# Performance work log

Measured on AMD Instinct MI355X. Metric: run time of the kernel, lower is better.

Reference implementation:

```python
import jax, jax.numpy as jnp
import numpy as np

NUM_JOINT_TYPES = 17
SINKHORN_ITERS = 50
TAU = 0.05
LAMBDA_RES = 0.5
LLOYD_ITERS = 10


def _sqdist(a, b):
    # squared euclidean distances [n, m] (== torch.cdist(...,p=2)**2)
    d = jnp.sum(a * a, -1)[:, None] + jnp.sum(b * b, -1)[None, :] - 2.0 * (a @ b.T)
    return jnp.maximum(d, 0.0)


def _kmeans_centroids(key, positions, k):
    # k-means++ init followed by LLOYD_ITERS Lloyd steps; result is a fixed
    # spatial prior (detached in the original), so stop_gradient at the end.
    n = positions.shape[0]
    key, k0 = jax.random.split(key)
    i0 = jax.random.randint(k0, (), 0, n)
    cents = jnp.zeros((k, 2), positions.dtype).at[0].set(positions[i0])

    def pp_body(i, carry):
        cents, key = carry
        key, sub = jax.random.split(key)
        d = _sqdist(positions, cents)                       # [n, k]
        d = jnp.where(jnp.arange(k)[None, :] < i, d, jnp.inf)
        dmin = jnp.min(d, axis=1)
        probs = dmin / (jnp.sum(dmin) + 1e-8)
        idx = jax.random.categorical(sub, jnp.log(probs + 1e-12))
        return cents.at[i].set(positions[idx]), key

    cents, _ = jax.lax.fori_loop(1, k, pp_body, (cents, key))

    def lloyd_body(_, cents):
        assign = jnp.argmin(_sqdist(positions, cents), axis=1)  # [n]
        sums = jax.ops.segment_sum(positions, assign, num_segments=k)
        counts = jax.ops.segment_sum(jnp.ones((n,), positions.dtype), assign, num_segments=k)
        means = sums / jnp.maximum(counts, 1.0)[:, None]
        return jnp.where((counts > 0)[:, None], means, cents)

    cents = jax.lax.fori_loop(0, LLOYD_ITERS, lloyd_body, cents)
    return jax.lax.stop_gradient(cents)


def _sinkhorn(cost, n, k):
    # log-domain Sinkhorn-Knopp with one slack column
    n_slots = k * NUM_JOINT_TYPES
    log_K_ext = jnp.concatenate([-cost / TAU, jnp.zeros((n, 1), cost.dtype)], axis=1)
    tgt = jnp.ones((n_slots + 1,), cost.dtype).at[-1].set(float(max(n - n_slots, 1)))
    log_tgt = jnp.log(tgt)

    def step(carry, _):
        log_u, log_v = carry
        log_u = -jax.scipy.special.logsumexp(log_K_ext + log_v[None, :], axis=1)
        log_v = log_tgt - jax.scipy.special.logsumexp(log_K_ext + log_u[:, None], axis=0)
        return (log_u, log_v), None

    init = (jnp.zeros((n,), cost.dtype), jnp.zeros((n_slots + 1,), cost.dtype))
    (log_u, log_v), _ = jax.lax.scan(jax.checkpoint(step), init, None, length=SINKHORN_ITERS)
    T = jnp.exp(log_K_ext + log_u[:, None] + log_v[None, :])
    return T[:, :n_slots]


def setup_inputs() -> dict:
    key = jax.random.key(0)
    k1, k2, k3, k4, k5 = jax.random.split(key, 5)
    N, D, H, K_MAX, K = 20000, 256, 128, 128, 64
    emb = jax.random.normal(k1, (N, D), jnp.float32)
    emb = emb / jnp.linalg.norm(emb, axis=-1, keepdims=True)  # L2-normalised per docstring
    positions = jax.random.uniform(k2, (N, 2), jnp.float32)
    W1 = jax.random.normal(k3, (D, H), jnp.float32) / np.sqrt(D)
    b1 = jnp.zeros((H,), jnp.float32)
    prototype_pool = jax.random.normal(k4, (K_MAX, H), jnp.float32) * 0.5
    joint_types = jax.random.randint(k5, (N,), 0, NUM_JOINT_TYPES, jnp.int32)
    return {"embeddings": emb, "positions": positions, "W1": W1, "b1": b1,
            "prototype_pool": prototype_pool, "joint_types": joint_types, "k": K}


def reference(embeddings, positions, W1, b1, prototype_pool, joint_types, k):
    n = embeddings.shape[0]
    h = jax.nn.selu(embeddings @ W1 + b1)                    # node_encoder
    prototypes = prototype_pool[:k]                          # k <= k_max branch
    c_learned = _sqdist(h, prototypes)                       # [n, k]
    centroids = _kmeans_centroids(jax.random.key(42), positions, k)
    c_spatial = _sqdist(positions, centroids)                # [n, k]
    cost_pp = c_spatial + LAMBDA_RES * c_learned
    cost = jnp.repeat(cost_pp, NUM_JOINT_TYPES, axis=1)      # [n, k*17]
    slot_types = jnp.tile(jnp.arange(NUM_JOINT_TYPES), k)
    type_mask = joint_types[:, None] == slot_types[None, :]
    cost = jnp.where(type_mask, cost, 1e6)
    T = _sinkhorn(cost, n, k)                                # [n, k*17]
    logits = jnp.log(T.reshape(n, k, NUM_JOINT_TYPES).sum(axis=2) + 1e-8)
    return logits, T
```

## Files before the change

### kernel.cpp

```cpp
#include <hip/hip_runtime.h>

#define NPT 20000
#define DIMK 256
#define HD 128
#define KC 64
#define NT 17
#define NSLOT (KC*NT)
#define SINK_IT 50
#define NBLK 250
#define RPB 80
#define LGB 64
#define CPB 313

#define OFF_H     0
#define OFF_CL    (NPT*HD)
#define OFF_Q     (OFF_CL + NPT*KC)
#define OFF_LS    (OFF_Q + KC*NPT)
#define OFF_LOGU  (OFF_LS + NPT*KC)
#define OFF_ORDER (OFF_LOGU + NPT)
#define OFF_TSV   (OFF_ORDER + NPT)
#define OFF_OFFS  (OFF_TSV + NPT)
#define OFF_CENTS (OFF_OFFS + 32)
#define OFF_I0    (OFF_CENTS + 128)
#define OFF_SUB   (OFF_I0 + 32)
#define OFF_LLP   (OFF_SUB + 128)
#define OFF_PMB   (OFF_LLP + LGB*192)
#define OFF_PSB   (OFF_PMB + NBLK*3*64)
#define OFF_RUNT  (OFF_PSB + NBLK*3*64)
#define OFF_PLM   (OFF_RUNT + 768)
#define OFF_PLS   (OFF_PLM + 256)

__device__ __forceinline__ void tf2x32(unsigned k0, unsigned k1,
                                       unsigned x0, unsigned x1,
                                       unsigned& o0, unsigned& o1) {
  unsigned ks0 = k0, ks1 = k1, ks2 = k0 ^ k1 ^ 0x1BD11BDAu;
  x0 += ks0; x1 += ks1;
  const int rot[2][4] = {{13,15,26,6},{17,29,16,24}};
  unsigned ks[3] = {ks0, ks1, ks2};
  #pragma unroll
  for (int i = 0; i < 5; ++i) {
    #pragma unroll
    for (int r = 0; r < 4; ++r) {
      int rr = rot[i & 1][r];
      x0 += x1;
      x1 = (x1 << rr) | (x1 >> (32 - rr));
      x1 ^= x0;
    }
    x0 += ks[(i+1)%3];
    x1 += ks[(i+2)%3] + (unsigned)(i+1);
  }
  o0 = x0; o1 = x1;
}

__device__ __forceinline__ void lse_merge(float& m, float& s, float m2, float s2) {
  float mn = fmaxf(m, m2);
  s = s*__expf(m - mn) + s2*__expf(m2 - mn);
  m = mn;
}

__global__ void k_keys(unsigned* sub, int* i0p) {
  if (threadIdx.x != 0 || blockIdx.x != 0) return;
  unsigned key0 = 0u, key1 = 42u;
  unsigned c0, c1, s0, s1;
  tf2x32(key0, key1, 0u, 0u, c0, c1);
  tf2x32(key0, key1, 0u, 1u, s0, s1);
  key0 = c0; key1 = c1;
  unsigned k1a, k1b, k2a, k2b;
  tf2x32(s0, s1, 0u, 0u, k1a, k1b);
  tf2x32(s0, s1, 0u, 1u, k2a, k2b);
  unsigned h0, h1, l0, l1;
  tf2x32(k1a, k1b, 0u, 0u, h0, h1);
  tf2x32(k2a, k2b, 0u, 0u, l0, l1);
  unsigned hb = h0 ^ h1, lb = l0 ^ l1;
  unsigned span = 20000u;
  unsigned m1 = 65536u % span;
  unsigned mult = (unsigned)(((unsigned long long)m1 * m1) % span);
  unsigned off32 = (hb % span) * mult + (lb % span);
  *i0p = (int)(off32 % span);
  sub[0] = 0u; sub[1] = 0u;
  for (int i = 1; i < KC; ++i) {
    tf2x32(key0, key1, 0u, 0u, c0, c1);
    tf2x32(key0, key1, 0u, 1u, s0, s1);
    key0 = c0; key1 = c1;
    sub[2*i] = s0; sub[2*i+1] = s1;
  }
}

__global__ __launch_bounds__(256) void k_gumbel(const unsigned* __restrict__ sub,
                                                float* __restrict__ Q) {
  int s = blockIdx.y + 1;
  int i = blockIdx.x * 256 + threadIdx.x;
  if (i >= NPT) return;
  unsigned o0, o1;
  tf2x32(sub[2*s], sub[2*s+1], 0u, (unsigned)i, o0, o1);
  unsigned bits = o0 ^ o1;
  unsigned fb = (bits >> 9) | 0x3f800000u;
  float u = __uint_as_float(fb) - 1.0f;
  if (u == 0.0f) u = 1.17549435e-38f;
  Q[(size_t)s*NPT + i] = -1.0f / logf(u);
}

__global__ __launch_bounds__(256) void k_gemm(const float* __restrict__ emb,
                                              const float* __restrict__ W1,
                                              const float* __restrict__ b1,
                                              float* __restrict__ h) {
  __shared__ float As[64][64];
  __shared__ float Bs[64][HD];
  const int m0 = blockIdx.x * 64;
  const int tid = threadIdx.x;
  const int tx = tid & 31;
  const int ty = tid >> 5;
  float acc[8][4];
  #pragma unroll
  for (int a = 0; a < 8; ++a)
    #pragma unroll
    for (int c = 0; c < 4; ++c) acc[a][c] = 0.f;

  for (int kc = 0; kc < DIMK; kc += 64) {
    #pragma unroll
    for (int it = 0; it < 4; ++it) {
      int f = it*256 + tid;
      int r = f >> 4;
      int kk = (f & 15) << 2;
      float4 v = make_float4(0.f,0.f,0.f,0.f);
      if (m0 + r < NPT)
        v = *(const float4*)(emb + (size_t)(m0 + r)*DIMK + kc + kk);
      As[kk+0][r] = v.x; As[kk+1][r] = v.y; As[kk+2][r] = v.z; As[kk+3][r] = v.w;
    }
    #pragma unroll
    for (int it = 0; it < 8; ++it) {
      int f = it*256 + tid;
      int kk = f >> 5;
      int cc = (f & 31) << 2;
      *(float4*)&Bs[kk][cc] = *(const float4*)(W1 + (size_t)(kc + kk)*HD + cc);
    }
    __syncthreads();
    #pragma unroll 8
    for (int kk = 0; kk < 64; ++kk) {
      float4 a0 = *(float4*)&As[kk][ty*8];
      float4 a1 = *(float4*)&As[kk][ty*8+4];
      float4 bb = *(float4*)&Bs[kk][tx*4];
      float av[8] = {a0.x,a0.y,a0.z,a0.w,a1.x,a1.y,a1.z,a1.w};
      float bv[4] = {bb.x,bb.y,bb.z,bb.w};
      #pragma unroll
      for (int a = 0; a < 8; ++a)
        #pragma unroll
        for (int c = 0; c < 4; ++c) acc[a][c] += av[a]*bv[c];
    }
    __syncthreads();
  }
  const float SC = 1.0507009873554805f, AL = 1.6732632423543772f;
  #pragma unroll
  for (int a = 0; a < 8; ++a) {
    int r = m0 + ty*8 + a;
    if (r >= NPT) continue;
    float4 o;
    float* po = &o.x;
    #pragma unroll
    for (int c = 0; c < 4; ++c) {
      float x = acc[a][c] + b1[tx*4 + c];
      float v = (x > 0.f) ? x : AL * expm1f(x);
      po[c] = SC * v;
    }
    *(float4*)(h + (size_t)r*HD + tx*4) = o;
  }
}

__global__ __launch_bounds__(256) void k_cl(const float* __restrict__ h,
                                            const float* __restrict__ protos,
                                            float* __restrict__ cl) {
  __shared__ float ps[KC][129];
  __shared__ float hs[4][HD];
  const int tid = threadIdx.x;
  #pragma unroll
  for (int it = 0; it < 32; ++it) {
    int f = it*256 + tid;
    ps[f >> 7][f & 127] = protos[f];
  }
  const int i0r = blockIdx.x * 4;
  for (int f = tid; f < 4*HD; f += 256) {
    int rr = f >> 7, d = f & 127;
    int gi = i0r + rr;
    hs[rr][d] = (gi < NPT) ? h[(size_t)gi*HD + d] : 0.f;
  }
  __syncthreads();
  const int j = tid & 63, rq = tid >> 6;
  const int gi = i0r + rq;
  if (gi < NPT) {
    float dot = 0.f, hh = 0.f, pp = 0.f;
    #pragma unroll 8
    for (int d = 0; d < HD; ++d) {
      float a = hs[rq][d], b = ps[j][d];
      dot += a*b; hh += a*a; pp += b*b;
    }
    float c = hh + pp - 2.f*dot;
    cl[(size_t)gi*KC + j] = fmaxf(c, 0.f);
  }
}

__global__ __launch_bounds__(512) void k_sort(const int* __restrict__ jt,
                                              int* order, int* tsv, int* offs) {
  __shared__ struct { unsigned cnt[512][NT]; int tot[NT]; int base[NT]; } sm;
  const int tid = threadIdx.x;
  const int CHS = 40;
  const int r0 = tid*CHS, r1 = min(NPT, r0 + CHS);
  for (int t = 0; t < NT; ++t) sm.cnt[tid][t] = 0;
  __syncthreads();
  for (int r = r0; r < r1; ++r) sm.cnt[tid][jt[r]]++;
  __syncthreads();
  if (tid < NT) {
    unsigned s = 0;
    for (int i = 0; i < 512; ++i) s += sm.cnt[i][tid];
    sm.tot[tid] = (int)s;
  }
  __syncthreads();
  if (tid == 0) {
    int acc = 0;
    for (int t = 0; t < NT; ++t) { sm.base[t] = acc; offs[t] = acc; acc += sm.tot[t]; }
    offs[NT] = acc;
  }
  __syncthreads();
  if (tid < NT) {
    unsigned run = (unsigned)sm.base[tid];
    for (int i = 0; i < 512; ++i) { unsigned c = sm.cnt[i][tid]; sm.cnt[i][tid] = run; run += c; }
  }
  __syncthreads();
  for (int r = r0; r < r1; ++r) {
    int t = jt[r];
    unsigned p = sm.cnt[tid][t]++;
    order[p] = r; tsv[p] = t;
  }
}

#define KPT 20
__global__ __launch_bounds__(1024, 1) void k_km(const float* __restrict__ pos,
                                                const int* __restrict__ i0p,
                                                const float* __restrict__ Q,
                                                float* centsg) {
  __shared__ float red[16];
  __shared__ int   redi[16];
  __shared__ int   bselsh;
  const int tid = threadIdx.x;
  const int lane = tid & 63, wv = tid >> 6;
  float dm[KPT];
  const int i0 = *i0p;
  float cx = pos[2*i0], cy = pos[2*i0+1];
  if (tid == 0) { centsg[0] = cx; centsg[1] = cy; }
  #pragma unroll
  for (int u = 0; u < KPT; ++u) dm[u] = 3.4e38f;
  for (int s = 1; s < KC; ++s) {
    const float* Qs = Q + (size_t)s*NPT;
    const float cc2 = cx*cx + cy*cy;
    float bsc = -3.4e38f; int bi = 0x7FFFFFFF;
    #pragma unroll
    for (int u = 0; u < KPT; ++u) {
      int i = tid + (u << 10);
      if (i < NPT) {
        float2 p = *(const float2*)(pos + 2*i);
        float d = fmaxf((p.x*p.x + p.y*p.y) + cc2 - 2.f*(p.x*cx + p.y*cy), 0.f);
        float nd = fminf(dm[u], d);
        dm[u] = nd;
        float sc = nd * Qs[i];
        if (sc > bsc || (sc == bsc && i < bi)) { bsc = sc; bi = i; }
      }
    }
    for (int o = 32; o; o >>= 1) {
      float osc = __shfl_xor(bsc, o, 64);
      int   oid = __shfl_xor(bi, o, 64);
      if (osc > bsc || (osc == bsc && oid < bi)) { bsc = osc; bi = oid; }
    }
    if (lane == 0) { red[wv] = bsc; redi[wv] = bi; }
    __syncthreads();
    if (tid == 0) {
      float bb = -3.4e38f; int bj = 0x7FFFFFFF;
      #pragma unroll
      for (int w = 0; w < 16; ++w) {
        float v2 = red[w]; int id2 = redi[w];
        if (v2 > bb || (v2 == bb && id2 < bj)) { bb = v2; bj = id2; }
      }
      bselsh = bj;
    }
    __syncthreads();
    const int sel = bselsh;
    cx = pos[2*sel]; cy = pos[2*sel+1];
    if (tid == 0) { centsg[2*s] = cx; centsg[2*s+1] = cy; }
    __syncthreads();
  }
}

__global__ __launch_bounds__(512) void k_lloyd(const float* __restrict__ pos,
                                               float* centsg, float* llp, int first) {
  const int b = blockIdx.x, tid = threadIdx.x, lane = tid & 63, wv = tid >> 6;
  __shared__ float cents[KC][2];
  __shared__ float comb[192];
  __shared__ float wpart[8][192];
  __shared__ int asg[CPB];
  if (tid < KC) { cents[tid][0] = centsg[2*tid]; cents[tid][1] = centsg[2*tid+1]; }
  __syncthreads();
  if (!first) {
    if (tid < 192) {
      float s = 0.f;
      for (int bb = 0; bb < LGB; ++bb) s += llp[bb*192 + tid];
      comb[tid] = s;
    }
    __syncthreads();
    if (tid < KC) {
      float cn = comb[128 + tid];
      if (cn > 0.f) {
        float dv = fmaxf(cn, 1.f);
        cents[tid][0] = comb[tid] / dv;
        cents[tid][1] = comb[64 + tid] / dv;
      }
    }
    __syncthreads();
    if (b == 0 && tid < KC) {
      centsg[2*tid] = cents[tid][0]; centsg[2*tid+1] = cents[tid][1];
    }
  }
  const int base = b*CPB;
  const int pcnt = max(0, min(NPT - base, CPB));
  if (tid < pcnt) {
    int i = base + tid;
    float x = pos[2*i], y = pos[2*i+1];
    float bd = 3.4e38f; int bj = 0;
    #pragma unroll 4
    for (int j = 0; j < KC; ++j) {
      float cx = cents[j][0], cy = cents[j][1];
      float d = (x*x + y*y) + (cx*cx + cy*cy) - 2.f*(x*cx + y*cy);
      d = fmaxf(d, 0.f);
      if (d < bd) { bd = d; bj = j; }
    }
    asg[tid] = bj;
  }
  __syncthreads();
  {
    int r0 = 40*wv, r1 = min(pcnt, r0 + 40);
    float sx = 0.f, sy = 0.f, cn = 0.f;
    for (int r = r0; r < r1; ++r) {
      int a = asg[r]; int i = base + r;
      float x = pos[2*i], y = pos[2*i+1];
      if (lane == a) { sx += x; sy += y; cn += 1.f; }
    }
    wpart[wv][lane] = sx; wpart[wv][64+lane] = sy; wpart[wv][128+lane] = cn;
  }
  __syncthreads();
  if (tid < 192) {
    float s = 0.f;
    #pragma unroll
    for (int w8 = 0; w8 < 8; ++w8) s += wpart[w8][tid];
    llp[b*192 + tid] = s;
  }
}

__global__ __launch_bounds__(512) void k_cb(const float* __restrict__ pos,
                                            const float* __restrict__ cl,
                                            const int* __restrict__ order,
                                            const int* __restrict__ tsv,
                                            const float* __restrict__ centsg,
                                            const float* __restrict__ llp,
                                            float* __restrict__ Ls, int* runT) {
  const int b = blockIdx.x, tid = threadIdx.x, lane = tid & 63, wv = tid >> 6;
  __shared__ float cents[KC][2];
  __shared__ float comb[192];
  if (tid < KC) { cents[tid][0] = centsg[2*tid]; cents[tid][1] = centsg[2*tid+1]; }
  __syncthreads();
  if (tid < 192) {
    float s = 0.f;
    for (int bb = 0; bb < LGB; ++bb) s += llp[bb*192 + tid];
    comb[tid] = s;
  }
  __syncthreads();
  if (tid < KC) {
    float cn = comb[128 + tid];
    if (cn > 0.f) {
      float dv = fmaxf(cn, 1.f);
      cents[tid][0] = comb[tid] / dv;
      cents[tid][1] = comb[64 + tid] / dv;
    }
  }
  if (tid == 0) {
    int nrun = 0, prev = -1;
    int rt[3] = {-1,-1,-1};
    for (int u = 0; u < RPB; ++u) {
      int t = tsv[b*RPB + u];
      if (t != prev) { if (nrun < 3) rt[nrun] = t; nrun++; prev = t; }
    }
    runT[b*3+0] = rt[0]; runT[b*3+1] = rt[1]; runT[b*3+2] = rt[2];
  }
  __syncthreads();
  #pragma unroll
  for (int k = 0; k < 10; ++k) {
    int ii = b*RPB + wv*10 + k;
    int od = order[ii];
    float x = pos[2*od], y = pos[2*od+1];
    float cx = cents[lane][0], cy = cents[lane][1];
    float cs = fmaxf((x*x + y*y) + (cx*cx + cy*cy) - 2.f*(x*cx + y*cy), 0.f);
    float cle = cl[(size_t)od*KC + lane];
    Ls[(size_t)ii*KC + lane] = -(cs + 0.5f*cle) / 0.05f;
  }
}

template<int FIRST>
__global__ __launch_bounds__(512) void k_sink(const float* __restrict__ Ls,
                                              float* __restrict__ logu,
                                              const int* __restrict__ offs,
                                              const int* __restrict__ runT,
                                              const int* __restrict__ tsv,
                                              float* __restrict__ PMb, float* __restrict__ PSb,
                                              float* __restrict__ PLm, float* __restrict__ PLs) {
  const int b = blockIdx.x, tid = threadIdx.x, lane = tid & 63, wv = tid >> 6;
  __shared__ float lvs[3][64];
  __shared__ float wpm[8][2][64], wps[8][2][64];
  __shared__ int   wri[8][2];
  __shared__ float plmw[8], plsw[8];
  __shared__ float lvl_sh;
  const int rt0 = runT[b*3+0], rt1 = runT[b*3+1], rt2 = runT[b*3+2];

  if (!FIRST) {
    if (wv < 3) {
      int t = (wv == 0) ? rt0 : ((wv == 1) ? rt1 : rt2);
      if (t >= 0) {
        float m = -3.4e38f, s = 0.f;
        int bb0 = offs[t] / RPB, bb1 = (offs[t+1] - 1) / RPB;
        for (int bb = bb0; bb <= bb1; ++bb) {
          #pragma unroll
          for (int q = 0; q < 3; ++q) {
            if (runT[bb*3+q] == t)
              lse_merge(m, s, PMb[(bb*3+q)*64 + lane], PSb[(bb*3+q)*64 + lane]);
          }
        }
        lvs[wv][lane] = -(__logf(s) + m);
      }
    } else if (wv == 3) {
      float m = -3.4e38f, s = 0.f;
      for (int bb = lane; bb < NBLK; bb += 64) lse_merge(m, s, PLm[bb], PLs[bb]);
      for (int o = 32; o; o >>= 1) {
        float m2 = __shfl_xor(m, o, 64), s2 = __shfl_xor(s, o, 64);
        lse_merge(m, s, m2, s2);
      }
      if (lane == 0) lvl_sh = logf((float)(NPT - NSLOT)) - (__logf(s) + m);
    }
    __syncthreads();
  }
  const float lvl = FIRST ? 0.f : lvl_sh;

  float am0 = -3.4e38f, as0 = 0.f, am1 = -3.4e38f, as1 = 0.f;
  int r0i = -1, r1i = -1;
  float lm = -3.4e38f, lss = 0.f;
  #pragma unroll
  for (int k = 0; k < 10; ++k) {
    int ii = b*RPB + wv*10 + k;
    int t = tsv[ii];
    int rq = (t == rt0) ? 0 : ((t == rt1) ? 1 : 2);
    float lvv = FIRST ? 0.f : lvs[rq][lane];
    float Lv = Ls[(size_t)ii*KC + lane];
    float x = Lv + lvv;
    float m = x;
    for (int o = 32; o; o >>= 1) m = fmaxf(m, __shfl_xor(m, o, 64));
    m = fmaxf(m, lvl);
    float e = __expf(x - m);
    for (int o = 32; o; o >>= 1) e += __shfl_xor(e, o, 64);
    e += __expf(lvl - m);
    float lu = -(__logf(e) + m);
    if (lane == 0) logu[ii] = lu;
    float cv = Lv + lu;
    if (r0i < 0 || rq == r0i) { r0i = rq; lse_merge(am0, as0, cv, 1.0f); }
    else                      { r1i = rq; lse_merge(am1, as1, cv, 1.0f); }
    lse_merge(lm, lss, lu, 1.0f);
  }
  wpm[wv][0][lane] = am0; wps[wv][0][lane] = as0;
  wpm[wv][1][lane] = am1; wps[wv][1][lane] = as1;
  if (lane == 0) { wri[wv][0] = r0i; wri[wv][1] = r1i; plmw[wv] = lm; plsw[wv] = lss; }
  __syncthreads();
  if (wv < 3) {
    float m = -3.4e38f, s = 0.f;
    for (int w8 = 0; w8 < 8; ++w8) {
      if (wri[w8][0] == wv) lse_merge(m, s, wpm[w8][0][lane], wps[w8][0][lane]);
      if (wri[w8][1] == wv) lse_merge(m, s, wpm[w8][1][lane], wps[w8][1][lane]);
    }
    PMb[(b*3+wv)*64 + lane] = m; PSb[(b*3+wv)*64 + lane] = s;
  } else if (wv == 3 && lane == 0) {
    float m = -3.4e38f, s = 0.f;
    #pragma unroll
    for (int w8 = 0; w8 < 8; ++w8) lse_merge(m, s, plmw[w8], plsw[w8]);
    PLm[b] = m; PLs[b] = s;
  }
}

__global__ __launch_bounds__(512) void k_fin(const float* __restrict__ Ls,
                                             const float* __restrict__ logu,
                                             const int* __restrict__ offs,
                                             const int* __restrict__ runT,
                                             const int* __restrict__ tsv,
                                             const int* __restrict__ order,
                                             const float* __restrict__ PMb,
                                             const float* __restrict__ PSb,
                                             float* __restrict__ vals) {
  const int b = blockIdx.x, tid = threadIdx.x, lane = tid & 63, wv = tid >> 6;
  __shared__ float lvs[3][64];
  const int rt0 = runT[b*3+0], rt1 = runT[b*3+1], rt2 = runT[b*3+2];
  if (wv < 3) {
    int t = (wv == 0) ? rt0 : ((wv == 1) ? rt1 : rt2);
    if (t >= 0) {
      float m = -3.4e38f, s = 0.f;
      int bb0 = offs[t] / RPB, bb1 = (offs[t+1] - 1) / RPB;
      for (int bb = bb0; bb <= bb1; ++bb) {
        #pragma unroll
        for (int q = 0; q < 3; ++q) {
          if (runT[bb*3+q] == t)
            lse_merge(m, s, PMb[(bb*3+q)*64 + lane], PSb[(bb*3+q)*64 + lane]);
        }
      }
      lvs[wv][lane] = -(__logf(s) + m);
    }
  }
  __syncthreads();
  #pragma unroll
  for (int k = 0; k < 10; ++k) {
    int ii = b*RPB + wv*10 + k;
    int t = tsv[ii];
    int rq = (t == rt0) ? 0 : ((t == rt1) ? 1 : 2);
    vals[(size_t)order[ii]*KC + lane] =
        __expf(Ls[(size_t)ii*KC + lane] + lvs[rq][lane] + logu[ii]);
  }
}

__global__ __launch_bounds__(256) void k_T(const float* __restrict__ vals,
                                           const int* __restrict__ jt,
                                           float* __restrict__ T) {
  __shared__ float v[KC];
  const int i = blockIdx.x;
  const int tid = threadIdx.x;
  if (tid < KC) v[tid] = vals[(size_t)i*KC + tid];
  __syncthreads();
  const int t = jt[i];
  for (int e = tid; e < NSLOT; e += 256) {
    int j = e / NT;
    int tt = e - j*NT;
    T[(size_t)i*NSLOT + e] = (tt == t) ? v[j] : 0.0f;
  }
}

__global__ __launch_bounds__(256) void k_logits(float* logits) {
  int idx = blockIdx.x*256 + threadIdx.x;
  if (idx < NPT*KC) logits[idx] = logf(logits[idx] + 1e-8f);
}

extern "C" void kernel_launch(void* const* d_in, const int* in_sizes, int n_in,
                              void* d_out, int out_size, void* d_ws, size_t ws_size,
                              hipStream_t stream) {
  const float* emb    = (const float*)d_in[0];
  const float* pos    = (const float*)d_in[1];
  const float* W1     = (const float*)d_in[2];
  const float* b1     = (const float*)d_in[3];
  const float* protos = (const float*)d_in[4];
  const int*   jt     = (const int*)d_in[5];

  float* out  = (float*)d_out;
  float* vals = out;
  float* T    = out + (size_t)NPT*KC;
  float* TS   = T;

  unsigned* sub = (unsigned*)(TS + OFF_SUB);
  int* i0p    = (int*)(TS + OFF_I0);
  int* order  = (int*)(TS + OFF_ORDER);
  int* tsv    = (int*)(TS + OFF_TSV);
  int* offs   = (int*)(TS + OFF_OFFS);
  int* runT   = (int*)(TS + OFF_RUNT);
  float* centsg = TS + OFF_CENTS;
  float* llp  = TS + OFF_LLP;
  float* Ls   = TS + OFF_LS;
  float* logu = TS + OFF_LOGU;
  float* PMb  = TS + OFF_PMB;
  float* PSb  = TS + OFF_PSB;
  float* PLm  = TS + OFF_PLM;
  float* PLs  = TS + OFF_PLS;

  hipLaunchKernelGGL(k_keys, dim3(1), dim3(64), 0, stream, sub, i0p);
  hipLaunchKernelGGL(k_gumbel, dim3((NPT + 255)/256, KC - 1), dim3(256), 0, stream,
                     sub, TS + OFF_Q);
  hipLaunchKernelGGL(k_gemm, dim3((NPT + 63)/64), dim3(256), 0, stream,
                     emb, W1, b1, TS + OFF_H);
  hipLaunchKernelGGL(k_cl, dim3((NPT + 3)/4), dim3(256), 0, stream,
                     TS + OFF_H, protos, TS + OFF_CL);
  hipLaunchKernelGGL(k_sort, dim3(1), dim3(512), 0, stream, jt, order, tsv, offs);
  hipLaunchKernelGGL(k_km, dim3(1), dim3(1024), 0, stream,
                     pos, i0p, TS + OFF_Q, centsg);

  for (int it = 0; it < 10; ++it)
    hipLaunchKernelGGL(k_lloyd, dim3(LGB), dim3(512), 0, stream,
                       pos, centsg, llp, (it == 0) ? 1 : 0);

  hipLaunchKernelGGL(k_cb, dim3(NBLK), dim3(512), 0, stream,
                     pos, TS + OFF_CL, order, tsv, centsg, llp, Ls, runT);

  hipLaunchKernelGGL(k_sink<1>, dim3(NBLK), dim3(512), 0, stream,
                     Ls, logu, offs, runT, tsv, PMb, PSb, PLm, PLs);
  for (int it = 1; it < SINK_IT; ++it)
    hipLaunchKernelGGL(k_sink<0>, dim3(NBLK), dim3(512), 0, stream,
                       Ls, logu, offs, runT, tsv, PMb, PSb, PLm, PLs);

  hipLaunchKernelGGL(k_fin, dim3(NBLK), dim3(512), 0, stream,
                     Ls, logu, offs, runT, tsv, order, PMb, PSb, vals);

  hipLaunchKernelGGL(k_T, dim3(NPT), dim3(256), 0, stream, vals, jt, T);
  hipLaunchKernelGGL(k_logits, dim3((NPT*KC + 255)/256), dim3(256), 0, stream, vals);
}
```

Before: 1.762 ms.

## Merge k-means++ init, GEMM+cost, and sort into one heterogeneous front kernel

```diff
diff --git a/kernel.cpp b/kernel.cpp
--- a/kernel.cpp
+++ b/kernel.cpp
@@ -11,6 +11,8 @@
 #define RPB 80
 #define LGB 64
 #define CPB 313
+#define GEB 313
+#define FBLK (1 + GEB + 1)
 
 #define OFF_H     0
 #define OFF_CL    (NPT*HD)
@@ -100,191 +102,184 @@
   Q[(size_t)s*NPT + i] = -1.0f / logf(u);
 }
 
-__global__ __launch_bounds__(256) void k_gemm(const float* __restrict__ emb,
-                                              const float* __restrict__ W1,
-                                              const float* __restrict__ b1,
-                                              float* __restrict__ h) {
-  __shared__ float As[64][64];
-  __shared__ float Bs[64][HD];
-  const int m0 = blockIdx.x * 64;
-  const int tid = threadIdx.x;
-  const int tx = tid & 31;
-  const int ty = tid >> 5;
-  float acc[8][4];
-  #pragma unroll
-  for (int a = 0; a < 8; ++a)
-    #pragma unroll
-    for (int c = 0; c < 4; ++c) acc[a][c] = 0.f;
-
-  for (int kc = 0; kc < DIMK; kc += 64) {
-    #pragma unroll
-    for (int it = 0; it < 4; ++it) {
-      int f = it*256 + tid;
-      int r = f >> 4;
-      int kk = (f & 15) << 2;
-      float4 v = make_float4(0.f,0.f,0.f,0.f);
-      if (m0 + r < NPT)
-        v = *(const float4*)(emb + (size_t)(m0 + r)*DIMK + kc + kk);
-      As[kk+0][r] = v.x; As[kk+1][r] = v.y; As[kk+2][r] = v.z; As[kk+3][r] = v.w;
-    }
-    #pragma unroll
-    for (int it = 0; it < 8; ++it) {
-      int f = it*256 + tid;
-      int kk = f >> 5;
-      int cc = (f & 31) << 2;
-      *(float4*)&Bs[kk][cc] = *(const float4*)(W1 + (size_t)(kc + kk)*HD + cc);
-    }
-    __syncthreads();
-    #pragma unroll 8
-    for (int kk = 0; kk < 64; ++kk) {
-      float4 a0 = *(float4*)&As[kk][ty*8];
-      float4 a1 = *(float4*)&As[kk][ty*8+4];
-      float4 bb = *(float4*)&Bs[kk][tx*4];
-      float av[8] = {a0.x,a0.y,a0.z,a0.w,a1.x,a1.y,a1.z,a1.w};
-      float bv[4] = {bb.x,bb.y,bb.z,bb.w};
-      #pragma unroll
-      for (int a = 0; a < 8; ++a)
-        #pragma unroll
-        for (int c = 0; c < 4; ++c) acc[a][c] += av[a]*bv[c];
-    }
-    __syncthreads();
-  }
-  const float SC = 1.0507009873554805f, AL = 1.6732632423543772f;
-  #pragma unroll
-  for (int a = 0; a < 8; ++a) {
-    int r = m0 + ty*8 + a;
-    if (r >= NPT) continue;
-    float4 o;
-    float* po = &o.x;
-    #pragma unroll
-    for (int c = 0; c < 4; ++c) {
-      float x = acc[a][c] + b1[tx*4 + c];
-      float v = (x > 0.f) ? x : AL * expm1f(x);
-      po[c] = SC * v;
-    }
-    *(float4*)(h + (size_t)r*HD + tx*4) = o;
-  }
-}
-
-__global__ __launch_bounds__(256) void k_cl(const float* __restrict__ h,
-                                            const float* __restrict__ protos,
-                                            float* __restrict__ cl) {
-  __shared__ float ps[KC][129];
-  __shared__ float hs[4][HD];
-  const int tid = threadIdx.x;
-  #pragma unroll
-  for (int it = 0; it < 32; ++it) {
-    int f = it*256 + tid;
-    ps[f >> 7][f & 127] = protos[f];
-  }
-  const int i0r = blockIdx.x * 4;
-  for (int f = tid; f < 4*HD; f += 256) {
-    int rr = f >> 7, d = f & 127;
-    int gi = i0r + rr;
-    hs[rr][d] = (gi < NPT) ? h[(size_t)gi*HD + d] : 0.f;
-  }
-  __syncthreads();
-  const int j = tid & 63, rq = tid >> 6;
-  const int gi = i0r + rq;
-  if (gi < NPT) {
-    float dot = 0.f, hh = 0.f, pp = 0.f;
-    #pragma unroll 8
-    for (int d = 0; d < HD; ++d) {
-      float a = hs[rq][d], b = ps[j][d];
-      dot += a*b; hh += a*a; pp += b*b;
-    }
-    float c = hh + pp - 2.f*dot;
-    cl[(size_t)gi*KC + j] = fmaxf(c, 0.f);
-  }
-}
-
-__global__ __launch_bounds__(512) void k_sort(const int* __restrict__ jt,
-                                              int* order, int* tsv, int* offs) {
-  __shared__ struct { unsigned cnt[512][NT]; int tot[NT]; int base[NT]; } sm;
-  const int tid = threadIdx.x;
-  const int CHS = 40;
-  const int r0 = tid*CHS, r1 = min(NPT, r0 + CHS);
-  for (int t = 0; t < NT; ++t) sm.cnt[tid][t] = 0;
-  __syncthreads();
-  for (int r = r0; r < r1; ++r) sm.cnt[tid][jt[r]]++;
-  __syncthreads();
-  if (tid < NT) {
-    unsigned s = 0;
-    for (int i = 0; i < 512; ++i) s += sm.cnt[i][tid];
-    sm.tot[tid] = (int)s;
-  }
-  __syncthreads();
-  if (tid == 0) {
-    int acc = 0;
-    for (int t = 0; t < NT; ++t) { sm.base[t] = acc; offs[t] = acc; acc += sm.tot[t]; }
-    offs[NT] = acc;
-  }
-  __syncthreads();
-  if (tid < NT) {
-    unsigned run = (unsigned)sm.base[tid];
-    for (int i = 0; i < 512; ++i) { unsigned c = sm.cnt[i][tid]; sm.cnt[i][tid] = run; run += c; }
-  }
-  __syncthreads();
-  for (int r = r0; r < r1; ++r) {
-    int t = jt[r];
-    unsigned p = sm.cnt[tid][t]++;
-    order[p] = r; tsv[p] = t;
-  }
-}
+union FrontSM {
+  struct { float red[16]; int redi[16]; int bsel; } km;
+  struct { float As[64][64]; float Bs[64][HD]; } ge;
+  struct { float ht[64][HD]; float ps[64][HD]; } c2;
+  struct { unsigned cnt[512][NT]; int tot[NT]; int base[NT]; } srt;
+};
 
 #define KPT 20
-__global__ __launch_bounds__(1024, 1) void k_km(const float* __restrict__ pos,
+__global__ __launch_bounds__(1024) void k_front(const float* __restrict__ pos,
                                                 const int* __restrict__ i0p,
                                                 const float* __restrict__ Q,
-                                                float* centsg) {
-  __shared__ float red[16];
-  __shared__ int   redi[16];
-  __shared__ int   bselsh;
-  const int tid = threadIdx.x;
+                                                float* centsg,
+                                                const float* __restrict__ emb,
+                                                const float* __restrict__ W1,
+                                                const float* __restrict__ b1,
+                                                const float* __restrict__ protos,
+                                                float* __restrict__ cl,
+                                                const int* __restrict__ jt,
+                                                int* order, int* tsv, int* offs) {
+  __shared__ FrontSM sm;
+  const int b = blockIdx.x, tid = threadIdx.x;
   const int lane = tid & 63, wv = tid >> 6;
-  float dm[KPT];
-  const int i0 = *i0p;
-  float cx = pos[2*i0], cy = pos[2*i0+1];
-  if (tid == 0) { centsg[0] = cx; centsg[1] = cy; }
-  #pragma unroll
-  for (int u = 0; u < KPT; ++u) dm[u] = 3.4e38f;
-  for (int s = 1; s < KC; ++s) {
-    const float* Qs = Q + (size_t)s*NPT;
-    const float cc2 = cx*cx + cy*cy;
-    float bsc = -3.4e38f; int bi = 0x7FFFFFFF;
+
+  if (b == 0) {
+    float dm[KPT];
+    const int i0 = *i0p;
+    float cx = pos[2*i0], cy = pos[2*i0+1];
+    if (tid == 0) { centsg[0] = cx; centsg[1] = cy; }
     #pragma unroll
-    for (int u = 0; u < KPT; ++u) {
-      int i = tid + (u << 10);
-      if (i < NPT) {
-        float2 p = *(const float2*)(pos + 2*i);
-        float d = fmaxf((p.x*p.x + p.y*p.y) + cc2 - 2.f*(p.x*cx + p.y*cy), 0.f);
-        float nd = fminf(dm[u], d);
-        dm[u] = nd;
-        float sc = nd * Qs[i];
-        if (sc > bsc || (sc == bsc && i < bi)) { bsc = sc; bi = i; }
-      }
-    }
-    for (int o = 32; o; o >>= 1) {
-      float osc = __shfl_xor(bsc, o, 64);
-      int   oid = __shfl_xor(bi, o, 64);
-      if (osc > bsc || (osc == bsc && oid < bi)) { bsc = osc; bi = oid; }
-    }
-    if (lane == 0) { red[wv] = bsc; redi[wv] = bi; }
+    for (int u = 0; u < KPT; ++u) dm[u] = 3.4e38f;
+    for (int s = 1; s < KC; ++s) {
+      const float* Qs = Q + (size_t)s*NPT;
+      const float cc2 = cx*cx + cy*cy;
+      float bsc = -3.4e38f; int bi = 0x7FFFFFFF;
+      #pragma unroll
+      for (int u = 0; u < KPT; ++u) {
+        int i = tid + (u << 10);
+        if (i < NPT) {
+          float2 p = *(const float2*)(pos + 2*i);
+          float d = fmaxf((p.x*p.x + p.y*p.y) + cc2 - 2.f*(p.x*cx + p.y*cy), 0.f);
+          float nd = fminf(dm[u], d);
+          dm[u] = nd;
+          float sc = nd * Qs[i];
+          if (sc > bsc || (sc == bsc && i < bi)) { bsc = sc; bi = i; }
+        }
+      }
+      for (int o = 32; o; o >>= 1) {
+        float osc = __shfl_xor(bsc, o, 64);
+        int   oid = __shfl_xor(bi, o, 64);
+        if (osc > bsc || (osc == bsc && oid < bi)) { bsc = osc; bi = oid; }
+      }
+      if (lane == 0) { sm.km.red[wv] = bsc; sm.km.redi[wv] = bi; }
+      __syncthreads();
+      if (tid == 0) {
+        float bb = -3.4e38f; int bj = 0x7FFFFFFF;
+        #pragma unroll
+        for (int w = 0; w < 16; ++w) {
+          float v2 = sm.km.red[w]; int id2 = sm.km.redi[w];
+          if (v2 > bb || (v2 == bb && id2 < bj)) { bb = v2; bj = id2; }
+        }
+        sm.km.bsel = bj;
+      }
+      __syncthreads();
+      const int sel = sm.km.bsel;
+      cx = pos[2*sel]; cy = pos[2*sel+1];
+      if (tid == 0) { centsg[2*s] = cx; centsg[2*s+1] = cy; }
+      __syncthreads();
+    }
+  } else if (b <= GEB) {
+    const int m0 = (b - 1) * 64;
+    const int tx = tid & 31, ty = (tid >> 5) & 7;
+    float acc[8][4];
+    #pragma unroll
+    for (int a = 0; a < 8; ++a)
+      #pragma unroll
+      for (int c = 0; c < 4; ++c) acc[a][c] = 0.f;
+
+    for (int kc = 0; kc < DIMK; kc += 64) {
+      if (tid < 256) {
+        #pragma unroll
+        for (int it = 0; it < 4; ++it) {
+          int f = it*256 + tid;
+          int r = f >> 4;
+          int kk = (f & 15) << 2;
+          float4 v = make_float4(0.f,0.f,0.f,0.f);
+          if (m0 + r < NPT)
+            v = *(const float4*)(emb + (size_t)(m0 + r)*DIMK + kc + kk);
+          sm.ge.As[kk+0][r] = v.x; sm.ge.As[kk+1][r] = v.y;
+          sm.ge.As[kk+2][r] = v.z; sm.ge.As[kk+3][r] = v.w;
+        }
+        #pragma unroll
+        for (int it = 0; it < 8; ++it) {
+          int f = it*256 + tid;
+          int kk = f >> 5;
+          int cc = (f & 31) << 2;
+          *(float4*)&sm.ge.Bs[kk][cc] = *(const float4*)(W1 + (size_t)(kc + kk)*HD + cc);
+        }
+      }
+      __syncthreads();
+      if (tid < 256) {
+        #pragma unroll 8
+        for (int kk = 0; kk < 64; ++kk) {
+          float4 a0 = *(float4*)&sm.ge.As[kk][ty*8];
+          float4 a1 = *(float4*)&sm.ge.As[kk][ty*8+4];
+          float4 bb = *(float4*)&sm.ge.Bs[kk][tx*4];
+          float av[8] = {a0.x,a0.y,a0.z,a0.w,a1.x,a1.y,a1.z,a1.w};
+          float bv[4] = {bb.x,bb.y,bb.z,bb.w};
+          #pragma unroll
+          for (int a = 0; a < 8; ++a)
+            #pragma unroll
+            for (int c = 0; c < 4; ++c) acc[a][c] += av[a]*bv[c];
+        }
+      }
+      __syncthreads();
+    }
+    if (tid < 256) {
+      const float SC = 1.0507009873554805f, AL = 1.6732632423543772f;
+      #pragma unroll
+      for (int a = 0; a < 8; ++a) {
+        int r = ty*8 + a;
+        #pragma unroll
+        for (int c = 0; c < 4; ++c) {
+          float x = acc[a][c] + b1[tx*4 + c];
+          float v = (x > 0.f) ? x : AL * expm1f(x);
+          sm.c2.ht[r][tx*4 + c] = SC * v;
+        }
+      }
+    }
+    for (int f = tid; f < KC*HD; f += 1024)
+      sm.c2.ps[f >> 7][f & 127] = protos[f];
+    __syncthreads();
+    #pragma unroll
+    for (int q = 0; q < 4; ++q) {
+      int p = tid + (q << 10);
+      int r = p >> 6, j = p & 63;
+      int gi = m0 + r;
+      if (gi < NPT) {
+        float dot = 0.f, hh = 0.f, pp = 0.f;
+        #pragma unroll 8
+        for (int d = 0; d < HD; ++d) {
+          float a = sm.c2.ht[r][d], bb = sm.c2.ps[j][d];
+          dot += a*bb; hh += a*a; pp += bb*bb;
+        }
+        float c = hh + pp - 2.f*dot;
+        cl[(size_t)gi*KC + j] = fmaxf(c, 0.f);
+      }
+    }
+  } else {
+    const int CHS = 40;
+    const int r0 = tid*CHS, r1 = min(NPT, r0 + CHS);
+    if (tid < 512) for (int t = 0; t < NT; ++t) sm.srt.cnt[tid][t] = 0;
+    __syncthreads();
+    if (tid < 512) for (int r = r0; r < r1; ++r) sm.srt.cnt[tid][jt[r]]++;
+    __syncthreads();
+    if (tid < NT) {
+      unsigned s = 0;
+      for (int i = 0; i < 512; ++i) s += sm.srt.cnt[i][tid];
+      sm.srt.tot[tid] = (int)s;
+    }
     __syncthreads();
     if (tid == 0) {
-      float bb = -3.4e38f; int bj = 0x7FFFFFFF;
-      #pragma unroll
-      for (int w = 0; w < 16; ++w) {
-        float v2 = red[w]; int id2 = redi[w];
-        if (v2 > bb || (v2 == bb && id2 < bj)) { bb = v2; bj = id2; }
-      }
-      bselsh = bj;
-    }
-    __syncthreads();
-    const int sel = bselsh;
-    cx = pos[2*sel]; cy = pos[2*sel+1];
-    if (tid == 0) { centsg[2*s] = cx; centsg[2*s+1] = cy; }
-    __syncthreads();
+      int acc = 0;
+      for (int t = 0; t < NT; ++t) { sm.srt.base[t] = acc; offs[t] = acc; acc += sm.srt.tot[t]; }
+      offs[NT] = acc;
+    }
+    __syncthreads();
+    if (tid < NT) {
+      unsigned run = (unsigned)sm.srt.base[tid];
+      for (int i = 0; i < 512; ++i) { unsigned c = sm.srt.cnt[i][tid]; sm.srt.cnt[i][tid] = run; run += c; }
+    }
+    __syncthreads();
+    if (tid < 512) {
+      for (int r = r0; r < r1; ++r) {
+        int t = jt[r];
+        unsigned p = sm.srt.cnt[tid][t]++;
+        order[p] = r; tsv[p] = t;
+      }
+    }
   }
 }
 
@@ -525,7 +520,7 @@
   }
 }
 
-__global__ __launch_bounds__(256) void k_T(const float* __restrict__ vals,
+__global__ __launch_bounds__(256) void k_T(float* __restrict__ vals,
                                            const int* __restrict__ jt,
                                            float* __restrict__ T) {
   __shared__ float v[KC];
@@ -539,11 +534,7 @@
     int tt = e - j*NT;
     T[(size_t)i*NSLOT + e] = (tt == t) ? v[j] : 0.0f;
   }
-}
-
-__global__ __launch_bounds__(256) void k_logits(float* logits) {
-  int idx = blockIdx.x*256 + threadIdx.x;
-  if (idx < NPT*KC) logits[idx] = logf(logits[idx] + 1e-8f);
+  if (tid < KC) vals[(size_t)i*KC + tid] = logf(v[tid] + 1e-8f);
 }
 
 extern "C" void kernel_launch(void* const* d_in, const int* in_sizes, int n_in,
@@ -579,13 +570,10 @@
   hipLaunchKernelGGL(k_keys, dim3(1), dim3(64), 0, stream, sub, i0p);
   hipLaunchKernelGGL(k_gumbel, dim3((NPT + 255)/256, KC - 1), dim3(256), 0, stream,
                      sub, TS + OFF_Q);
-  hipLaunchKernelGGL(k_gemm, dim3((NPT + 63)/64), dim3(256), 0, stream,
-                     emb, W1, b1, TS + OFF_H);
-  hipLaunchKernelGGL(k_cl, dim3((NPT + 3)/4), dim3(256), 0, stream,
-                     TS + OFF_H, protos, TS + OFF_CL);
-  hipLaunchKernelGGL(k_sort, dim3(1), dim3(512), 0, stream, jt, order, tsv, offs);
-  hipLaunchKernelGGL(k_km, dim3(1), dim3(1024), 0, stream,
-                     pos, i0p, TS + OFF_Q, centsg);
+  hipLaunchKernelGGL(k_front, dim3(FBLK), dim3(1024), 0, stream,
+                     pos, i0p, TS + OFF_Q, centsg,
+                     emb, W1, b1, protos, TS + OFF_CL,
+                     jt, order, tsv, offs);
 
   for (int it = 0; it < 10; ++it)
     hipLaunchKernelGGL(k_lloyd, dim3(LGB), dim3(512), 0, stream,
@@ -604,5 +592,4 @@
                      Ls, logu, offs, runT, tsv, order, PMb, PSb, vals);
 
   hipLaunchKernelGGL(k_T, dim3(NPT), dim3(256), 0, stream, vals, jt, T);
-  hipLaunchKernelGGL(k_logits, dim3((NPT*KC + 255)/256), dim3(256), 0, stream, vals);
-}
+}
```

Result: faster. 1.682 ms (-4.5%).
